# Kernel optimization log

Hardware: AMD Instinct MI355X
Metric: run time of the kernel (lower is better)

The kernel has to match this reference:

```python
import jax, jax.numpy as jnp
import numpy as np

NL, NQ, FD, HD, NH = 6, 128, 256, 512, 8
NC, B, T, H, W = 6, 1, 1, 48, 120
PPF = 24 // 6  # points_per_face
P = PPF * PPF * 6  # code emits (num_points//6)^2 points per face = 96 total
NPARAM, NTYPE, NATTR = 11, 10, 3
PMIN = np.array([-50., -50., -5., -15., -15., -5., -5., -3.14, 0.5, 0.5, 0.5], np.float32)
PMAX = np.array([50., 50., 5., 15., 15., 5., 5., 3.14, 10., 5., 3.], np.float32)


def _box_template():
    off = np.linspace(-0.4, 0.4, PPF).astype(np.float32)
    pts = []
    for axis in range(3):  # -x,+x,-y,+y,-z,+z faces, same order as torch code
        for s in (-0.5, 0.5):
            rem = [a for a in range(3) if a != axis]
            for i in range(PPF):
                for j in range(PPF):
                    p = [0.0, 0.0, 0.0]
                    p[axis] = s
                    p[rem[0]] = off[i]
                    p[rem[1]] = off[j]
                    pts.append(p)
    return np.asarray(pts, np.float32)  # [P,3]

TPL = _box_template()


def _mlp2(x, w1, b1, w2, b2):
    return jax.nn.relu(x @ w1.T + b1) @ w2.T + b2


def _ln(x, g, b):
    m = x.mean(-1, keepdims=True)
    v = ((x - m) ** 2).mean(-1, keepdims=True)
    return (x - m) * jax.lax.rsqrt(v + 1e-5) * g + b


def _mha(q, k, v, in_w, in_b, out_w, out_b):
    hd = HD // NH
    wq, wk, wv = jnp.split(in_w, 3, axis=0)
    bq, bk, bv = jnp.split(in_b, 3)
    def heads(x, w, b):
        y = x @ w.T + b
        return y.reshape(x.shape[0], x.shape[1], NH, hd).transpose(0, 2, 1, 3)
    Q, K, V = heads(q, wq, bq), heads(k, wk, bk), heads(v, wv, bv)
    a = jax.nn.softmax(jnp.einsum('bhqd,bhkd->bhqk', Q, K) * (hd ** -0.5), axis=-1)
    o = jnp.einsum('bhqk,bhkd->bhqd', a, V)
    o = o.transpose(0, 2, 1, 3).reshape(q.shape[0], q.shape[1], HD)
    return o @ out_w.T + out_b


def _sample_box_points(motion):
    # motion [B,N,11] -> [B,N,P,3]; indices: X0 Y1 Z2 .. YAW7 L8 W9 H10
    c = motion[..., 0:3]
    dims = motion[..., 8:11]
    yaw = motion[..., 7]
    p = TPL * dims[:, :, None, :]  # [B,N,P,3]
    cy, sy = jnp.cos(yaw)[..., None], jnp.sin(yaw)[..., None]
    xr = p[..., 0] * cy - p[..., 1] * sy
    yr = p[..., 0] * sy + p[..., 1] * cy
    return jnp.stack([xr, yr, p[..., 2]], -1) + c[:, :, None, :]


def _gather_aggregate(pts, features, proj):
    # pts [B,N,P,3]; features [NC,B,T,C,H,W]; proj [NC,3,4]
    Bb, N, Pp, _ = pts.shape
    NP = N * Pp
    hom = jnp.concatenate([pts, jnp.ones_like(pts[..., :1])], -1)
    feat_flat = features.reshape(NC, Bb, T, FD, H * W)
    acc = jnp.zeros((Bb, FD, NP), features.dtype)
    for cidx in range(NC):
        cam = jnp.einsum('ij,bnpj->bnpi', proj[cidx], hom)  # [B,N,P,3]
        z = cam[..., 2]
        zs = jnp.where(jnp.abs(z) > 1e-6, z, 1e-6)
        u = (cam[..., 0] / zs).reshape(Bb, NP)
        v = (cam[..., 1] / zs).reshape(Bb, NP)
        front = (z > 0).reshape(Bb, NP)
        u0, v0 = jnp.floor(u), jnp.floor(v)
        du, dv = u - u0, v - v0
        cam_acc = jnp.zeros((Bb, T, FD, NP), features.dtype)
        for (ui, vi, wgt) in ((u0, v0, (1 - du) * (1 - dv)),
                              (u0 + 1, v0, du * (1 - dv)),
                              (u0, v0 + 1, (1 - du) * dv),
                              (u0 + 1, v0 + 1, du * dv)):
            ok = front & (ui >= 0) & (ui <= W - 1) & (vi >= 0) & (vi <= H - 1)
            idx = (jnp.clip(vi, 0, H - 1) * W + jnp.clip(ui, 0, W - 1)).astype(jnp.int32)
            bidx = jnp.broadcast_to(idx[:, None, None, :], (Bb, T, FD, NP))
            g = jnp.take_along_axis(feat_flat[cidx], bidx, axis=-1)
            cam_acc = cam_acc + g * (wgt * ok)[:, None, None, :]
        acc = acc + cam_acc.mean(axis=1)  # mean over time
    agg = (acc / NC).reshape(Bb, FD, N, Pp).mean(-1)  # mean over cams and points
    return agg.transpose(0, 2, 1)  # [B,N,C]

_ga = jax.checkpoint(_gather_aggregate)


def _forward(features, proj, ego_states, queries0, param_min, param_max, motion_w1, motion_b1, motion_w2, motion_b2, type_w1, type_b1, type_w2, type_b2, attr_w1, attr_b1, attr_w2, attr_b2, fmlp_w1, fmlp_b1, fmlp_w2, fmlp_b2, sa_in_w, sa_in_b, sa_out_w, sa_out_b, fa_in_w, fa_in_b, fa_out_w, fa_out_b, ffn_w1, ffn_b1, ffn_w2, ffn_b2, ln1_g, ln1_b, ln2_g, ln2_b, ln3_g, ln3_b):
    Bb = features.shape[1]
    q = jnp.broadcast_to(queries0, (Bb, NQ, HD))
    preds = []
    for i in range(NL):
        motion = jax.nn.sigmoid(_mlp2(q, motion_w1, motion_b1, motion_w2, motion_b2)) * (param_max - param_min) + param_min
        tlog = _mlp2(q, type_w1, type_b1, type_w2, type_b2)
        attr = jax.nn.sigmoid(_mlp2(q, attr_w1, attr_b1, attr_w2, attr_b2))
        preds.append(jnp.concatenate([motion, tlog, attr], -1))
        if i == NL - 1:
            break  # last layer only predicts (layers[-1] unused, as in torch code)
        pts = _sample_box_points(motion)
        agg = _ga(pts, features, proj)
        feat_h = _mlp2(agg, fmlp_w1, fmlp_b1, fmlp_w2, fmlp_b2)
        x = _ln(q, ln1_g[i], ln1_b[i])
        x = x + _mha(x, x, x, sa_in_w[i], sa_in_b[i], sa_out_w[i], sa_out_b[i])
        x = _ln(x, ln2_g[i], ln2_b[i])
        x = x + _mha(x, feat_h, feat_h, fa_in_w[i], fa_in_b[i], fa_out_w[i], fa_out_b[i])
        x = _ln(x, ln3_g[i], ln3_b[i])
        q = x + _mlp2(x, ffn_w1[i], ffn_b1[i], ffn_w2[i], ffn_b2[i])
    return jnp.stack(preds)  # [NL,B,NQ,24]


def setup_inputs() -> dict:
    key = jax.random.key(0)
    ks = iter(jax.random.split(key, 64))
    def g(shape, s=0.02):
        return jax.random.normal(next(ks), shape, jnp.float32) * s
    fx, cx, cy = 40.0, W / 2.0, H / 2.0
    Ps = []
    for c in range(NC):
        th = 2.0 * np.pi * c / NC
        Rm = np.stack([np.array([-np.sin(th), np.cos(th), 0.0]),
                       np.array([0.0, 0.0, -1.0]),
                       np.array([np.cos(th), np.sin(th), 0.0])])
        K = np.array([[fx, 0.0, cx], [0.0, fx, cy], [0.0, 0.0, 1.0]])
        Pm = np.zeros((3, 4))
        Pm[:, :3] = K @ Rm
        Ps.append(Pm)
    inp = dict(
        features=jax.random.normal(next(ks), (NC, B, T, FD, H, W), jnp.float32),
        proj=jnp.asarray(np.asarray(Ps, np.float32)),
        ego_states=jax.random.normal(next(ks), (B, T, 5), jnp.float32),
        queries0=g((1, NQ, HD), 1.0),
        param_min=jnp.asarray(PMIN), param_max=jnp.asarray(PMAX),
        motion_w1=g((HD, HD)), motion_b1=jnp.zeros((HD,)),
        motion_w2=g((NPARAM, HD)), motion_b2=jnp.zeros((NPARAM,)),
        type_w1=g((HD, HD)), type_b1=jnp.zeros((HD,)),
        type_w2=g((NTYPE, HD)), type_b2=jnp.zeros((NTYPE,)),
        attr_w1=g((HD, HD)), attr_b1=jnp.zeros((HD,)),
        attr_w2=g((NATTR, HD)), attr_b2=jnp.zeros((NATTR,)),
        fmlp_w1=g((HD, FD)), fmlp_b1=jnp.zeros((HD,)),
        fmlp_w2=g((HD, HD)), fmlp_b2=jnp.zeros((HD,)),
        sa_in_w=g((NL, 3 * HD, HD)), sa_in_b=jnp.zeros((NL, 3 * HD)),
        sa_out_w=g((NL, HD, HD)), sa_out_b=jnp.zeros((NL, HD)),
        fa_in_w=g((NL, 3 * HD, HD)), fa_in_b=jnp.zeros((NL, 3 * HD)),
        fa_out_w=g((NL, HD, HD)), fa_out_b=jnp.zeros((NL, HD)),
        ffn_w1=g((NL, 4 * HD, HD)), ffn_b1=jnp.zeros((NL, 4 * HD)),
        ffn_w2=g((NL, HD, 4 * HD)), ffn_b2=jnp.zeros((NL, HD)),
        ln1_g=jnp.ones((NL, HD)), ln1_b=jnp.zeros((NL, HD)),
        ln2_g=jnp.ones((NL, HD)), ln2_b=jnp.zeros((NL, HD)),
        ln3_g=jnp.ones((NL, HD)), ln3_b=jnp.zeros((NL, HD)),
    )
    return inp


def reference(features, proj, ego_states, queries0, param_min, param_max, motion_w1, motion_b1, motion_w2, motion_b2, type_w1, type_b1, type_w2, type_b2, attr_w1, attr_b1, attr_w2, attr_b2, fmlp_w1, fmlp_b1, fmlp_w2, fmlp_b2, sa_in_w, sa_in_b, sa_out_w, sa_out_b, fa_in_w, fa_in_b, fa_out_w, fa_out_b, ffn_w1, ffn_b1, ffn_w2, ffn_b2, ln1_g, ln1_b, ln2_g, ln2_b, ln3_g, ln3_b):
    return _forward(features, proj, ego_states, queries0, param_min, param_max, motion_w1, motion_b1, motion_w2, motion_b2, type_w1, type_b1, type_w2, type_b2, attr_w1, attr_b1, attr_w2, attr_b2, fmlp_w1, fmlp_b1, fmlp_w2, fmlp_b2, sa_in_w, sa_in_b, sa_out_w, sa_out_b, fa_in_w, fa_in_b, fa_out_w, fa_out_b, ffn_w1, ffn_b1, ffn_w2, ffn_b2, ln1_g, ln1_b, ln2_g, ln2_b, ln3_g, ln3_b)
```

## Files before the change

kernel.cpp:

```cpp
#include <hip/hip_runtime.h>
#include <hip/hip_bf16.h>

typedef __hip_bfloat16 bf16;
typedef _Float16 h16;
typedef __attribute__((ext_vector_type(8))) _Float16 half8;
typedef __attribute__((ext_vector_type(4))) float f32x4;

#define NQ 128
#define HD 512
#define FD 256
#define NC 6
#define IMH 48
#define IMW 120
#define HW 5760

__device__ __forceinline__ half8 pack8(float4 x, float4 y) {
    half8 h;
    h[0] = (h16)x.x; h[1] = (h16)x.y; h[2] = (h16)x.z; h[3] = (h16)x.w;
    h[4] = (h16)y.x; h[5] = (h16)y.y; h[6] = (h16)y.z; h[7] = (h16)y.w;
    return h;
}

__global__ __launch_bounds__(256) void transpose_feat_k(const float* __restrict__ f,
                                                        bf16* __restrict__ ft)
{
    __shared__ float tile[32][33];
    int cam = blockIdx.z;
    int hw0 = blockIdx.x * 32, fd0 = blockIdx.y * 32;
    int tx = threadIdx.x, ty = threadIdx.y;
    const float* fb = f + (size_t)cam * FD * HW;
    for (int r = ty; r < 32; r += 8)
        tile[r][tx] = fb[(size_t)(fd0 + r) * HW + hw0 + tx];
    __syncthreads();
    bf16* fo = ft + (size_t)cam * HW * FD;
    for (int r = ty; r < 32; r += 8)
        fo[(size_t)(hw0 + r) * FD + fd0 + tx] = __float2bfloat16(tile[tx][r]);
}

__global__ __launch_bounds__(256) void cvt16_k(const float* __restrict__ src,
                                               h16* __restrict__ dst, int n)
{
    int i = blockIdx.x * 256 + threadIdx.x;
    if (i < n) dst[i] = (h16)src[i];
}

struct SwzDesc {
    const float* src[11];
    unsigned int chunkStart[12];
    unsigned int tileStart[11];
    int K[11];
};

__global__ __launch_bounds__(256) void swizzle2_k(SwzDesc d, h16* __restrict__ dst)
{
    __shared__ h16 fbuf[4096];
    int bid = blockIdx.x;
    int w = 0;
    while (bid >= (int)d.chunkStart[w + 1]) w++;
    int local = bid - (int)d.chunkStart[w];
    int Kk = d.K[w];
    int kc = Kk >> 6;
    int n64 = local / kc, kchunk = local - n64 * kc;
    int t = threadIdx.x;
    int r = t >> 2, q = t & 3;
    int ct = r >> 4, lr = r & 15;
    const float* srow = d.src[w] + (size_t)(n64 * 64 + r) * Kk + kchunk * 64;
#pragma unroll
    for (int p = 0; p < 4; p++) {
        int c = (q + p * 4) * 4;
        float4 u = *(const float4*)(srow + c);
        int ksl = c >> 5, kk = c & 31;
        h16* fp = &fbuf[(size_t)(((ksl * 4 + ct) * 64) + (kk >> 3) * 16 + lr) * 8 + (kk & 7)];
        fp[0] = (h16)u.x; fp[1] = (h16)u.y; fp[2] = (h16)u.z; fp[3] = (h16)u.w;
    }
    __syncthreads();
    int K32 = Kk >> 5;
#pragma unroll
    for (int i = 0; i < 2; i++) {
        int hidx = t + i * 256;
        int tl = hidx >> 6, within = hidx & 63;
        int ksl = tl >> 2, ctt = tl & 3;
        size_t tileg = (size_t)d.tileStart[w]
                     + ((size_t)n64 * K32 + (kchunk * 2 + ksl)) * 4 + ctt;
        *(half8*)(dst + tileg * 512 + within * 8) = *(const half8*)&fbuf[tl * 512 + within * 8];
    }
}

template<int CTN, int NSUM, bool A2SW, bool LNA>
__global__ __launch_bounds__(256) void gemm_sk4(
    const h16* __restrict__ A16, int lda, int sumStride,
    const float* __restrict__ A32,
    const float* __restrict__ lng, const float* __restrict__ lnb,
    float* __restrict__ lnout,
    const h16* __restrict__ A2_16, int a2Start,
    const h16* __restrict__ Wswz,
    const float* __restrict__ B0, const float* __restrict__ B1, const float* __restrict__ B2s,
    const float* __restrict__ R, int ldr,
    float* __restrict__ C32, h16* __restrict__ C16, int ldc,
    int K, int act)
{
    __shared__ float redu[CTN * 4 * 256];
    __shared__ float sst[64], sst2[64];
    int bx = blockIdx.x, by = blockIdx.y;
    int tid = threadIdx.x;
    int w = tid >> 6, l = tid & 63;
    int lr = l & 15, q4 = l >> 4;
    int m0 = by * 16;
    int n0 = bx * 16 * CTN;
    int row = m0 + lr;
    int K32 = K >> 5;
    int KQ = K32 >> 2;
    int ks0 = w * KQ;

    bool useA2 = A2SW && (bx >= a2Start);

    const float* arow32 = nullptr;
    float mean = 0.f, rstd = 1.f;
    if (LNA && !useA2) {
        arow32 = A32 + (size_t)row * K + q4 * 8;
        float s = 0.f, s2 = 0.f;
        for (int ks = ks0; ks < ks0 + KQ; ks++) {
            float4 u = *(const float4*)(arow32 + ks * 32);
            float4 v = *(const float4*)(arow32 + ks * 32 + 4);
            s  += u.x + u.y + u.z + u.w + v.x + v.y + v.z + v.w;
            s2 += u.x*u.x + u.y*u.y + u.z*u.z + u.w*u.w
                + v.x*v.x + v.y*v.y + v.z*v.z + v.w*v.w;
        }
        s  += __shfl_xor(s, 16);  s  += __shfl_xor(s, 32);
        s2 += __shfl_xor(s2, 16); s2 += __shfl_xor(s2, 32);
        if (q4 == 0) { sst[w * 16 + lr] = s; sst2[w * 16 + lr] = s2; }
        __syncthreads();
        float st = sst[lr] + sst[16 + lr] + sst[32 + lr] + sst[48 + lr];
        float st2 = sst2[lr] + sst2[16 + lr] + sst2[32 + lr] + sst2[48 + lr];
        mean = st * (1.0f / (float)K);
        float var = st2 * (1.0f / (float)K) - mean * mean;
        rstd = rsqrtf(var + 1e-5f);
    }

    const h16* arow16 = nullptr;
    if (useA2)       arow16 = A2_16 + (size_t)row * 512 + q4 * 8;
    else if (!LNA)   arow16 = A16 + (size_t)row * lda + q4 * 8;

    const h16* wbase[CTN];
#pragma unroll
    for (int ct = 0; ct < CTN; ct++) {
        int tct = (n0 >> 4) + ct;
        wbase[ct] = Wswz + (((size_t)(tct >> 2) * K32 * 4 + (tct & 3)) * 64 + l) * 8;
    }

    f32x4 acc[CTN];
#pragma unroll
    for (int ct = 0; ct < CTN; ct++) acc[ct] = (f32x4){0.f, 0.f, 0.f, 0.f};

    bool wrln = LNA && !useA2 && (bx == 0) && lnout;

#pragma unroll 4
    for (int ks = ks0; ks < ks0 + KQ; ks++) {
        half8 a;
        if (LNA && !useA2) {
            float4 u = *(const float4*)(arow32 + ks * 32);
            float4 v = *(const float4*)(arow32 + ks * 32 + 4);
            float4 g0 = *(const float4*)(lng + ks * 32 + q4 * 8);
            float4 g1 = *(const float4*)(lng + ks * 32 + q4 * 8 + 4);
            float4 b0 = *(const float4*)(lnb + ks * 32 + q4 * 8);
            float4 b1 = *(const float4*)(lnb + ks * 32 + q4 * 8 + 4);
            float4 o0, o1;
            o0.x = (u.x - mean) * rstd * g0.x + b0.x;
            o0.y = (u.y - mean) * rstd * g0.y + b0.y;
            o0.z = (u.z - mean) * rstd * g0.z + b0.z;
            o0.w = (u.w - mean) * rstd * g0.w + b0.w;
            o1.x = (v.x - mean) * rstd * g1.x + b1.x;
            o1.y = (v.y - mean) * rstd * g1.y + b1.y;
            o1.z = (v.z - mean) * rstd * g1.z + b1.z;
            o1.w = (v.w - mean) * rstd * g1.w + b1.w;
            if (wrln) {
                *(float4*)(lnout + (size_t)row * K + ks * 32 + q4 * 8)     = o0;
                *(float4*)(lnout + (size_t)row * K + ks * 32 + q4 * 8 + 4) = o1;
            }
            a = pack8(o0, o1);
        } else if (NSUM == 1) {
            a = *(const half8*)(arow16 + (size_t)ks * 32);
        } else {
            float s[8] = {0.f, 0.f, 0.f, 0.f, 0.f, 0.f, 0.f, 0.f};
#pragma unroll
            for (int j = 0; j < NSUM; j++) {
                half8 tt = *(const half8*)(arow16 + (size_t)j * sumStride + ks * 32);
#pragma unroll
                for (int e = 0; e < 8; e++) s[e] += (float)tt[e];
            }
#pragma unroll
            for (int e = 0; e < 8; e++) a[e] = (h16)s[e];
        }
#pragma unroll
        for (int ct = 0; ct < CTN; ct++) {
            half8 bfr = *(const half8*)(wbase[ct] + (size_t)ks * 2048);
            acc[ct] = __builtin_amdgcn_mfma_f32_16x16x32_f16(a, bfr, acc[ct], 0, 0, 0);
        }
    }

#pragma unroll
    for (int ct = 0; ct < CTN; ct++)
        *(f32x4*)&redu[(size_t)(w * CTN + ct) * 256 + l * 4] = acc[ct];
    __syncthreads();

    if (w < CTN) {
        int ct = w;
        f32x4 sum = *(const f32x4*)&redu[(size_t)ct * 256 + l * 4];
#pragma unroll
        for (int w2 = 1; w2 < 4; w2++) {
            f32x4 tt = *(const f32x4*)&redu[(size_t)(w2 * CTN + ct) * 256 + l * 4];
            sum[0] += tt[0]; sum[1] += tt[1]; sum[2] += tt[2]; sum[3] += tt[3];
        }
        int n = n0 + ct * 16 + lr;
        float bv;
        if (B1) { int sec = n >> 9, ni = n & 511;
                  bv = (sec == 0) ? B0[ni] : (sec == 1 ? B1[ni] : B2s[ni]); }
        else bv = B0[n];
#pragma unroll
        for (int r = 0; r < 4; r++) {
            int m = m0 + q4 * 4 + r;
            float v = sum[r] + bv;
            if (act) v = fmaxf(v, 0.f);
            if (R) v += R[(size_t)m * ldr + n];
            if (C32) C32[(size_t)m * ldc + n] = v;
            if (C16) C16[(size_t)m * ldc + n] = (h16)v;
        }
    }
}

__global__ __launch_bounds__(64) void heads2_k(const h16* __restrict__ hid16,
                                               const float* __restrict__ w2m, const float* __restrict__ b2m,
                                               const float* __restrict__ w2t, const float* __restrict__ b2t,
                                               const float* __restrict__ w2a, const float* __restrict__ b2a,
                                               const float* __restrict__ pmin, const float* __restrict__ pmax,
                                               float* __restrict__ out)
{
    int q = blockIdx.x, n = blockIdx.y, lane = threadIdx.x;
    const float* wr; float bv; int mode, sect;
    if (n < 11)      { sect = 0; wr = w2m + n * 512;        bv = b2m[n];      mode = 0; }
    else if (n < 21) { sect = 1; wr = w2t + (n - 11) * 512; bv = b2t[n - 11]; mode = 1; }
    else             { sect = 2; wr = w2a + (n - 21) * 512; bv = b2a[n - 21]; mode = 2; }
    half8 hv = *(const half8*)(hid16 + q * 1536 + sect * 512 + lane * 8);
    const float4* w4 = (const float4*)(wr + lane * 8);
    float4 c0 = w4[0], c1 = w4[1];
    float acc = (float)hv[0] * c0.x + (float)hv[1] * c0.y
              + (float)hv[2] * c0.z + (float)hv[3] * c0.w
              + (float)hv[4] * c1.x + (float)hv[5] * c1.y
              + (float)hv[6] * c1.z + (float)hv[7] * c1.w;
    for (int off = 32; off; off >>= 1) acc += __shfl_xor(acc, off);
    if (lane == 0) {
        float v = acc + bv;
        if (mode == 0)      v = (1.0f / (1.0f + __expf(-v))) * (pmax[n] - pmin[n]) + pmin[n];
        else if (mode == 2) v = 1.0f / (1.0f + __expf(-v));
        out[q * 24 + n] = v;
    }
}

__global__ __launch_bounds__(256) void attn_k(const float* __restrict__ qkv,
                                              h16* __restrict__ out16)
{
    __shared__ float KVl[128 * 68];
    __shared__ float Ql[32 * 68];
    __shared__ float Pl[32 * 128];
    int h = blockIdx.x >> 2, chunk = blockIdx.x & 3;
    int tid = threadIdx.x;

    for (int l = tid; l < 2048; l += 256) {
        int row = l >> 4, c4 = (l & 15) * 4;
        float4 v = *(const float4*)&qkv[row * 1536 + 512 + h * 64 + c4];
        *(float4*)&KVl[row * 68 + c4] = v;
    }
    for (int l = tid; l < 512; l += 256) {
        int row = l >> 4, c4 = (l & 15) * 4;
        float4 v = *(const float4*)&qkv[(chunk * 32 + row) * 1536 + h * 64 + c4];
        *(float4*)&Ql[row * 68 + c4] = v;
    }
    __syncthreads();

    int w = tid >> 6, j = tid & 63;
    for (int r8 = 0; r8 < 8; r8++) {
        int lr = w * 8 + r8;
        float s0 = 0.f, s1 = 0.f;
#pragma unroll
        for (int k4 = 0; k4 < 64; k4 += 4) {
            float4 qv  = *(const float4*)&Ql[lr * 68 + k4];
            float4 k0v = *(const float4*)&KVl[j * 68 + k4];
            float4 k1v = *(const float4*)&KVl[(j + 64) * 68 + k4];
            s0 += qv.x * k0v.x + qv.y * k0v.y + qv.z * k0v.z + qv.w * k0v.w;
            s1 += qv.x * k1v.x + qv.y * k1v.y + qv.z * k1v.z + qv.w * k1v.w;
        }
        s0 *= 0.125f; s1 *= 0.125f;
        float m = fmaxf(s0, s1);
        for (int off = 32; off; off >>= 1) m = fmaxf(m, __shfl_xor(m, off));
        float e0 = __expf(s0 - m), e1 = __expf(s1 - m);
        float sm = e0 + e1;
        for (int off = 32; off; off >>= 1) sm += __shfl_xor(sm, off);
        float inv = 1.0f / sm;
        Pl[lr * 128 + j]      = e0 * inv;
        Pl[lr * 128 + j + 64] = e1 * inv;
    }
    __syncthreads();

    for (int l = tid; l < 2048; l += 256) {
        int row = l >> 4, c4 = (l & 15) * 4;
        float4 v = *(const float4*)&qkv[row * 1536 + 1024 + h * 64 + c4];
        KVl[(c4 + 0) * 132 + row] = v.x;
        KVl[(c4 + 1) * 132 + row] = v.y;
        KVl[(c4 + 2) * 132 + row] = v.z;
        KVl[(c4 + 3) * 132 + row] = v.w;
    }
    __syncthreads();

    int d = tid & 63, w2 = tid >> 6;
    for (int r8 = 0; r8 < 8; r8++) {
        int lr = w2 * 8 + r8;
        float o = 0.f;
#pragma unroll
        for (int j4 = 0; j4 < 128; j4 += 4) {
            float4 pv = *(const float4*)&Pl[lr * 128 + j4];
            float4 vv = *(const float4*)&KVl[d * 132 + j4];
            o += pv.x * vv.x + pv.y * vv.y + pv.z * vv.z + pv.w * vv.w;
        }
        out16[(chunk * 32 + lr) * 512 + h * 64 + d] = (h16)o;
    }
}

__device__ __forceinline__ float bflo(unsigned u) {
    union { unsigned i; float f; } c; c.i = u << 16; return c.f;
}
__device__ __forceinline__ float bfhi(unsigned u) {
    union { unsigned i; float f; } c; c.i = u & 0xffff0000u; return c.f;
}

__global__ __launch_bounds__(256) void gather_k(const bf16* __restrict__ ft,
                                                const float* __restrict__ proj,
                                                const float* __restrict__ preds,
                                                h16* __restrict__ agg16)
{
    __shared__ float mo[11];
    __shared__ int   goff[384];
    __shared__ float gw[384];
    __shared__ int   cnt;
    __shared__ float part[8][256];
    int n = blockIdx.x, cam = blockIdx.y, tid = threadIdx.x;
    if (tid == 0) cnt = 0;
    if (tid < 11) mo[tid] = preds[n * 24 + tid];
    __syncthreads();

    if (tid < 96) {
        int p = tid;
        float dd0 = mo[8], dd1 = mo[9], dd2 = mo[10];
        float c0 = mo[0], c1 = mo[1], c2 = mo[2];
        float sy, cy;
        sincosf(mo[7], &sy, &cy);
        int face = p >> 4, axis = face >> 1;
        float sgn = (face & 1) ? 0.5f : -0.5f;
        float offi = -0.4f + (float)((p >> 2) & 3) * (0.8f / 3.0f);
        float offj = -0.4f + (float)(p & 3) * (0.8f / 3.0f);
        float t0, t1, t2;
        if (axis == 0)      { t0 = sgn;  t1 = offi; t2 = offj; }
        else if (axis == 1) { t0 = offi; t1 = sgn;  t2 = offj; }
        else                { t0 = offi; t1 = offj; t2 = sgn;  }
        float px = t0 * dd0, py = t1 * dd1, pz = t2 * dd2;
        float X = px * cy - py * sy + c0;
        float Y = px * sy + py * cy + c1;
        float Z = pz + c2;
        const float* P = proj + cam * 12;
        float cu = P[0] * X + P[1] * Y + P[2] * Z + P[3];
        float cv = P[4] * X + P[5] * Y + P[6] * Z + P[7];
        float cz = P[8] * X + P[9] * Y + P[10] * Z + P[11];
        float zs = (fabsf(cz) > 1e-6f) ? cz : 1e-6f;
        float u = cu / zs, v = cv / zs;
        bool front = cz > 0.0f;
        float u0 = floorf(u), v0 = floorf(v);
        float du = u - u0, dv = v - v0;
        float us[4] = {u0, u0 + 1.0f, u0, u0 + 1.0f};
        float vs[4] = {v0, v0, v0 + 1.0f, v0 + 1.0f};
        float wt[4] = {(1.0f - du) * (1.0f - dv), du * (1.0f - dv),
                       (1.0f - du) * dv, du * dv};
        int   myoff[4]; float myw[4]; int k = 0;
#pragma unroll
        for (int t = 0; t < 4; t++) {
            bool ok = front && (us[t] >= 0.0f) && (us[t] <= 119.0f)
                            && (vs[t] >= 0.0f) && (vs[t] <= 47.0f)
                            && (wt[t] > 0.0f);
            if (ok) {
                myoff[k] = ((int)vs[t] * IMW + (int)us[t]) * FD;
                myw[k]   = wt[t];
                k++;
            }
        }
        if (k) {
            int base = atomicAdd(&cnt, k);
            for (int s = 0; s < k; s++) { goff[base + s] = myoff[s]; gw[base + s] = myw[s]; }
        }
    }
    __syncthreads();
    int C = cnt;
    h16* slab = agg16 + (size_t)cam * 32768 + n * 256;
    if (C == 0) { slab[tid] = (h16)0.f; return; }

    int g8  = (tid & 31) * 8;
    int row = tid >> 5;
    const bf16* fb = ft + (size_t)cam * HW * FD + g8;
    float acc[8] = {0.f, 0.f, 0.f, 0.f, 0.f, 0.f, 0.f, 0.f};
    for (int e = row; e < C; e += 8) {
        float w = gw[e];
        uint4 rv = *(const uint4*)(fb + goff[e]);
        acc[0] += w * bflo(rv.x); acc[1] += w * bfhi(rv.x);
        acc[2] += w * bflo(rv.y); acc[3] += w * bfhi(rv.y);
        acc[4] += w * bflo(rv.z); acc[5] += w * bfhi(rv.z);
        acc[6] += w * bflo(rv.w); acc[7] += w * bfhi(rv.w);
    }
#pragma unroll
    for (int j = 0; j < 8; j++) part[row][g8 + j] = acc[j];
    __syncthreads();
    float s = 0.f;
#pragma unroll
    for (int r = 0; r < 8; r++) s += part[r][tid];
    slab[tid] = (h16)(s * (1.0f / 576.0f));
}

extern "C" void kernel_launch(void* const* d_in, const int* in_sizes, int n_in,
                              void* d_out, int out_size, void* d_ws, size_t ws_size,
                              hipStream_t stream)
{
    const float* features  = (const float*)d_in[0];
    const float* proj      = (const float*)d_in[1];
    const float* queries0  = (const float*)d_in[3];
    const float* pmin      = (const float*)d_in[4];
    const float* pmax      = (const float*)d_in[5];
    const float* motion_w1 = (const float*)d_in[6];
    const float* motion_b1 = (const float*)d_in[7];
    const float* motion_w2 = (const float*)d_in[8];
    const float* motion_b2 = (const float*)d_in[9];
    const float* type_w1   = (const float*)d_in[10];
    const float* type_b1   = (const float*)d_in[11];
    const float* type_w2   = (const float*)d_in[12];
    const float* type_b2   = (const float*)d_in[13];
    const float* attr_w1   = (const float*)d_in[14];
    const float* attr_b1   = (const float*)d_in[15];
    const float* attr_w2   = (const float*)d_in[16];
    const float* attr_b2   = (const float*)d_in[17];
    const float* fmlp_w1   = (const float*)d_in[18];
    const float* fmlp_b1   = (const float*)d_in[19];
    const float* fmlp_w2   = (const float*)d_in[20];
    const float* fmlp_b2   = (const float*)d_in[21];
    const float* sa_in_w   = (const float*)d_in[22];
    const float* sa_in_b   = (const float*)d_in[23];
    const float* sa_out_w  = (const float*)d_in[24];
    const float* sa_out_b  = (const float*)d_in[25];
    const float* fa_in_w   = (const float*)d_in[26];
    const float* fa_in_b   = (const float*)d_in[27];
    const float* fa_out_w  = (const float*)d_in[28];
    const float* fa_out_b  = (const float*)d_in[29];
    const float* ffn_w1    = (const float*)d_in[30];
    const float* ffn_b1    = (const float*)d_in[31];
    const float* ffn_w2    = (const float*)d_in[32];
    const float* ffn_b2    = (const float*)d_in[33];
    const float* ln1_g     = (const float*)d_in[34];
    const float* ln1_b     = (const float*)d_in[35];
    const float* ln2_g     = (const float*)d_in[36];
    const float* ln2_b     = (const float*)d_in[37];
    const float* ln3_g     = (const float*)d_in[38];
    const float* ln3_b     = (const float*)d_in[39];
    float* out = (float*)d_out;

    char* p = (char*)d_ws;
    bf16* feat_t = (bf16*)p;   p += (size_t)NC * HW * FD * 2;
    h16* swz     = (h16*)p;    p += (size_t)51456 * 512 * 2;
    h16* q016    = (h16*)p;    p += 65536 * 2;
    h16* hid16   = (h16*)p;    p += 196608 * 2;
    h16* agg16   = (h16*)p;    p += 196608 * 2;
    h16* fmlph16 = (h16*)p;    p += 65536 * 2;
    h16* feath16 = (h16*)p;    p += 65536 * 2;
    h16* attnb16 = (h16*)p;    p += 65536 * 2;
    h16* ffnh16  = (h16*)p;    p += 262144 * 2;
    h16* qn16    = (h16*)p;    p += 65536 * 2;
    float* qkv   = (float*)p;  p += 196608 * 4;
    float* lnx   = (float*)p;  p += 65536 * 4;
    float* x1    = (float*)p;  p += 65536 * 4;
    float* x2    = (float*)p;  p += 65536 * 4;
    float* qn32  = (float*)p;  p += 65536 * 4;

    SwzDesc sd;
    const float* srcs[11] = {motion_w1, type_w1, attr_w1, fmlp_w1, fmlp_w2,
                             sa_in_w, sa_out_w, fa_in_w, fa_out_w, ffn_w1, ffn_w2};
    int Ks[11]    = {512, 512, 512, 256, 512, 512, 512, 512, 512, 512, 2048};
    int tiles[11] = {512, 512, 512, 256, 512, 9216, 3072, 9216, 3072, 12288, 12288};
    unsigned int cumT = 0, cumC = 0;
    for (int i = 0; i < 11; i++) {
        sd.src[i] = srcs[i]; sd.K[i] = Ks[i];
        sd.tileStart[i] = cumT; sd.chunkStart[i] = cumC;
        cumT += tiles[i]; cumC += tiles[i] >> 3;
    }
    sd.chunkStart[11] = cumC;

    swizzle2_k<<<6432, 256, 0, stream>>>(sd, swz);
    cvt16_k<<<256, 256, 0, stream>>>(queries0, q016, 65536);
    transpose_feat_k<<<dim3(180, 8, 6), dim3(32, 8), 0, stream>>>(features, feat_t);

    const h16* sw_heads = swz;
    const h16* sw_fmlp1 = swz + 786432;
    const h16* sw_fmlp2 = swz + 917504;
    const h16* sw_sain  = swz + 1179648;
    const h16* sw_saout = swz + 5898240;
    const h16* sw_fain  = swz + 7471104;
    const h16* sw_faout = swz + 12189696;
    const h16* sw_ffn1  = swz + 13762560;
    const h16* sw_ffn2  = swz + 20054016;

    const h16*   q16 = q016;
    const float* q32 = queries0;

    for (int i = 0; i < 6; i++) {
        gemm_sk4<2, 1, false, false><<<dim3(48, 8), 256, 0, stream>>>(
            q16, 512, 0, nullptr, nullptr, nullptr, nullptr, nullptr, 0,
            sw_heads, motion_b1, type_b1, attr_b1, nullptr, 0,
            nullptr, hid16, 1536, 512, 1);
        heads2_k<<<dim3(128, 24), 64, 0, stream>>>(hid16, motion_w2, motion_b2,
                                                   type_w2, type_b2, attr_w2, attr_b2,
                                                   pmin, pmax, out + i * 3072);
        if (i == 5) break;

        gather_k<<<dim3(128, 6), 256, 0, stream>>>(feat_t, proj, out + i * 3072, agg16);
        gemm_sk4<1, 6, false, false><<<dim3(32, 8), 256, 0, stream>>>(
            agg16, 256, 32768, nullptr, nullptr, nullptr, nullptr, nullptr, 0,
            sw_fmlp1, fmlp_b1, nullptr, nullptr, nullptr, 0,
            nullptr, fmlph16, 512, 256, 1);
        gemm_sk4<1, 1, false, false><<<dim3(32, 8), 256, 0, stream>>>(
            fmlph16, 512, 0, nullptr, nullptr, nullptr, nullptr, nullptr, 0,
            sw_fmlp2, fmlp_b2, nullptr, nullptr, nullptr, 0,
            nullptr, feath16, 512, 512, 0);

        gemm_sk4<2, 1, false, true><<<dim3(48, 8), 256, 0, stream>>>(
            nullptr, 0, 0, q32, ln1_g + i * 512, ln1_b + i * 512, lnx, nullptr, 0,
            sw_sain + (size_t)i * 786432, sa_in_b + i * 1536, nullptr, nullptr,
            nullptr, 0, qkv, nullptr, 1536, 512, 0);
        attn_k<<<32, 256, 0, stream>>>(qkv, attnb16);
        gemm_sk4<1, 1, false, false><<<dim3(32, 8), 256, 0, stream>>>(
            attnb16, 512, 0, nullptr, nullptr, nullptr, nullptr, nullptr, 0,
            sw_saout + (size_t)i * 262144, sa_out_b + i * 512, nullptr, nullptr,
            lnx, 512, x1, nullptr, 512, 512, 0);

        gemm_sk4<2, 1, true, true><<<dim3(48, 8), 256, 0, stream>>>(
            nullptr, 0, 0, x1, ln2_g + i * 512, ln2_b + i * 512, lnx, feath16, 16,
            sw_fain + (size_t)i * 786432, fa_in_b + i * 1536, nullptr, nullptr,
            nullptr, 0, qkv, nullptr, 1536, 512, 0);
        attn_k<<<32, 256, 0, stream>>>(qkv, attnb16);
        gemm_sk4<1, 1, false, false><<<dim3(32, 8), 256, 0, stream>>>(
            attnb16, 512, 0, nullptr, nullptr, nullptr, nullptr, nullptr, 0,
            sw_faout + (size_t)i * 262144, fa_out_b + i * 512, nullptr, nullptr,
            lnx, 512, x2, nullptr, 512, 512, 0);

        gemm_sk4<2, 1, false, true><<<dim3(64, 8), 256, 0, stream>>>(
            nullptr, 0, 0, x2, ln3_g + i * 512, ln3_b + i * 512, lnx, nullptr, 0,
            sw_ffn1 + (size_t)i * 1048576, ffn_b1 + i * 2048, nullptr, nullptr,
            nullptr, 0, nullptr, ffnh16, 2048, 512, 1);
        gemm_sk4<1, 1, false, false><<<dim3(32, 8), 256, 0, stream>>>(
            ffnh16, 2048, 0, nullptr, nullptr, nullptr, nullptr, nullptr, 0,
            sw_ffn2 + (size_t)i * 1048576, ffn_b2 + i * 512, nullptr, nullptr,
            lnx, 512, qn32, qn16, 512, 2048, 0);

        q16 = qn16;
        q32 = qn32;
    }
}
```

Measured before the change: 863.2 us.

## Drop weight pre-swizzle pass and read fp32 weights directly in GEMMs

Removes the upfront kernel that converted every weight matrix to fp16 in an MFMA-tiled layout. The GEMM now loads fp32 rows straight from the original weights and packs them to fp16 in registers. This saves one large conversion pass over all weights, but each GEMM reads twice the bytes with a less coalesced, row-strided pattern. Some weights are reused across the 6 iterations, so they are now converted repeatedly.

```diff
diff --git a/kernel.cpp b/kernel.cpp
--- a/kernel.cpp
+++ b/kernel.cpp
@@ -44,48 +44,6 @@
     if (i < n) dst[i] = (h16)src[i];
 }
 
-struct SwzDesc {
-    const float* src[11];
-    unsigned int chunkStart[12];
-    unsigned int tileStart[11];
-    int K[11];
-};
-
-__global__ __launch_bounds__(256) void swizzle2_k(SwzDesc d, h16* __restrict__ dst)
-{
-    __shared__ h16 fbuf[4096];
-    int bid = blockIdx.x;
-    int w = 0;
-    while (bid >= (int)d.chunkStart[w + 1]) w++;
-    int local = bid - (int)d.chunkStart[w];
-    int Kk = d.K[w];
-    int kc = Kk >> 6;
-    int n64 = local / kc, kchunk = local - n64 * kc;
-    int t = threadIdx.x;
-    int r = t >> 2, q = t & 3;
-    int ct = r >> 4, lr = r & 15;
-    const float* srow = d.src[w] + (size_t)(n64 * 64 + r) * Kk + kchunk * 64;
-#pragma unroll
-    for (int p = 0; p < 4; p++) {
-        int c = (q + p * 4) * 4;
-        float4 u = *(const float4*)(srow + c);
-        int ksl = c >> 5, kk = c & 31;
-        h16* fp = &fbuf[(size_t)(((ksl * 4 + ct) * 64) + (kk >> 3) * 16 + lr) * 8 + (kk & 7)];
-        fp[0] = (h16)u.x; fp[1] = (h16)u.y; fp[2] = (h16)u.z; fp[3] = (h16)u.w;
-    }
-    __syncthreads();
-    int K32 = Kk >> 5;
-#pragma unroll
-    for (int i = 0; i < 2; i++) {
-        int hidx = t + i * 256;
-        int tl = hidx >> 6, within = hidx & 63;
-        int ksl = tl >> 2, ctt = tl & 3;
-        size_t tileg = (size_t)d.tileStart[w]
-                     + ((size_t)n64 * K32 + (kchunk * 2 + ksl)) * 4 + ctt;
-        *(half8*)(dst + tileg * 512 + within * 8) = *(const half8*)&fbuf[tl * 512 + within * 8];
-    }
-}
-
 template<int CTN, int NSUM, bool A2SW, bool LNA>
 __global__ __launch_bounds__(256) void gemm_sk4(
     const h16* __restrict__ A16, int lda, int sumStride,
@@ -93,7 +51,7 @@
     const float* __restrict__ lng, const float* __restrict__ lnb,
     float* __restrict__ lnout,
     const h16* __restrict__ A2_16, int a2Start,
-    const h16* __restrict__ Wswz,
+    const float* __restrict__ W0f, const float* __restrict__ W1f, const float* __restrict__ W2f,
     const float* __restrict__ B0, const float* __restrict__ B1, const float* __restrict__ B2s,
     const float* __restrict__ R, int ldr,
     float* __restrict__ C32, h16* __restrict__ C16, int ldc,
@@ -141,11 +99,18 @@
     if (useA2)       arow16 = A2_16 + (size_t)row * 512 + q4 * 8;
     else if (!LNA)   arow16 = A16 + (size_t)row * lda + q4 * 8;
 
-    const h16* wbase[CTN];
+    const float* wrow[CTN];
 #pragma unroll
     for (int ct = 0; ct < CTN; ct++) {
-        int tct = (n0 >> 4) + ct;
-        wbase[ct] = Wswz + (((size_t)(tct >> 2) * K32 * 4 + (tct & 3)) * 64 + l) * 8;
+        int nb = n0 + ct * 16;
+        const float* ws;
+        if (W1f) {
+            int sec = nb >> 9, ni = nb & 511;
+            ws = (sec == 0 ? W0f : (sec == 1 ? W1f : W2f)) + (size_t)ni * K;
+        } else {
+            ws = W0f + (size_t)nb * K;
+        }
+        wrow[ct] = ws + (size_t)lr * K + q4 * 8;
     }
 
     f32x4 acc[CTN];
@@ -193,7 +158,10 @@
         }
 #pragma unroll
         for (int ct = 0; ct < CTN; ct++) {
-            half8 bfr = *(const half8*)(wbase[ct] + (size_t)ks * 2048);
+            const float* wp = wrow[ct] + (size_t)ks * 32;
+            float4 wu = *(const float4*)(wp);
+            float4 wv = *(const float4*)(wp + 4);
+            half8 bfr = pack8(wu, wv);
             acc[ct] = __builtin_amdgcn_mfma_f32_16x16x32_f16(a, bfr, acc[ct], 0, 0, 0);
         }
     }
@@ -468,7 +436,6 @@
 
     char* p = (char*)d_ws;
     bf16* feat_t = (bf16*)p;   p += (size_t)NC * HW * FD * 2;
-    h16* swz     = (h16*)p;    p += (size_t)51456 * 512 * 2;
     h16* q016    = (h16*)p;    p += 65536 * 2;
     h16* hid16   = (h16*)p;    p += 196608 * 2;
     h16* agg16   = (h16*)p;    p += 196608 * 2;
@@ -483,32 +450,8 @@
     float* x2    = (float*)p;  p += 65536 * 4;
     float* qn32  = (float*)p;  p += 65536 * 4;
 
-    SwzDesc sd;
-    const float* srcs[11] = {motion_w1, type_w1, attr_w1, fmlp_w1, fmlp_w2,
-                             sa_in_w, sa_out_w, fa_in_w, fa_out_w, ffn_w1, ffn_w2};
-    int Ks[11]    = {512, 512, 512, 256, 512, 512, 512, 512, 512, 512, 2048};
-    int tiles[11] = {512, 512, 512, 256, 512, 9216, 3072, 9216, 3072, 12288, 12288};
-    unsigned int cumT = 0, cumC = 0;
-    for (int i = 0; i < 11; i++) {
-        sd.src[i] = srcs[i]; sd.K[i] = Ks[i];
-        sd.tileStart[i] = cumT; sd.chunkStart[i] = cumC;
-        cumT += tiles[i]; cumC += tiles[i] >> 3;
-    }
-    sd.chunkStart[11] = cumC;
-
-    swizzle2_k<<<6432, 256, 0, stream>>>(sd, swz);
     cvt16_k<<<256, 256, 0, stream>>>(queries0, q016, 65536);
     transpose_feat_k<<<dim3(180, 8, 6), dim3(32, 8), 0, stream>>>(features, feat_t);
-
-    const h16* sw_heads = swz;
-    const h16* sw_fmlp1 = swz + 786432;
-    const h16* sw_fmlp2 = swz + 917504;
-    const h16* sw_sain  = swz + 1179648;
-    const h16* sw_saout = swz + 5898240;
-    const h16* sw_fain  = swz + 7471104;
-    const h16* sw_faout = swz + 12189696;
-    const h16* sw_ffn1  = swz + 13762560;
-    const h16* sw_ffn2  = swz + 20054016;
 
     const h16*   q16 = q016;
     const float* q32 = queries0;
@@ -516,7 +459,8 @@
     for (int i = 0; i < 6; i++) {
         gemm_sk4<2, 1, false, false><<<dim3(48, 8), 256, 0, stream>>>(
             q16, 512, 0, nullptr, nullptr, nullptr, nullptr, nullptr, 0,
-            sw_heads, motion_b1, type_b1, attr_b1, nullptr, 0,
+            motion_w1, type_w1, attr_w1,
+            motion_b1, type_b1, attr_b1, nullptr, 0,
             nullptr, hid16, 1536, 512, 1);
         heads2_k<<<dim3(128, 24), 64, 0, stream>>>(hid16, motion_w2, motion_b2,
                                                    type_w2, type_b2, attr_w2, attr_b2,
@@ -526,40 +470,48 @@
         gather_k<<<dim3(128, 6), 256, 0, stream>>>(feat_t, proj, out + i * 3072, agg16);
         gemm_sk4<1, 6, false, false><<<dim3(32, 8), 256, 0, stream>>>(
             agg16, 256, 32768, nullptr, nullptr, nullptr, nullptr, nullptr, 0,
-            sw_fmlp1, fmlp_b1, nullptr, nullptr, nullptr, 0,
+            fmlp_w1, nullptr, nullptr,
+            fmlp_b1, nullptr, nullptr, nullptr, 0,
             nullptr, fmlph16, 512, 256, 1);
         gemm_sk4<1, 1, false, false><<<dim3(32, 8), 256, 0, stream>>>(
             fmlph16, 512, 0, nullptr, nullptr, nullptr, nullptr, nullptr, 0,
-            sw_fmlp2, fmlp_b2, nullptr, nullptr, nullptr, 0,
+            fmlp_w2, nullptr, nullptr,
+            fmlp_b2, nullptr, nullptr, nullptr, 0,
             nullptr, feath16, 512, 512, 0);
 
         gemm_sk4<2, 1, false, true><<<dim3(48, 8), 256, 0, stream>>>(
             nullptr, 0, 0, q32, ln1_g + i * 512, ln1_b + i * 512, lnx, nullptr, 0,
-            sw_sain + (size_t)i * 786432, sa_in_b + i * 1536, nullptr, nullptr,
+            sa_in_w + (size_t)i * 1536 * 512, nullptr, nullptr,
+            sa_in_b + i * 1536, nullptr, nullptr,
             nullptr, 0, qkv, nullptr, 1536, 512, 0);
         attn_k<<<32, 256, 0, stream>>>(qkv, attnb16);
         gemm_sk4<1, 1, false, false><<<dim3(32, 8), 256, 0, stream>>>(
             attnb16, 512, 0, nullptr, nullptr, nullptr, nullptr, nullptr, 0,
-            sw_saout + (size_t)i * 262144, sa_out_b + i * 512, nullptr, nullptr,
+            sa_out_w + (size_t)i * 512 * 512, nullptr, nullptr,
+            sa_out_b + i * 512, nullptr, nullptr,
             lnx, 512, x1, nullptr, 512, 512, 0);
 
         gemm_sk4<2, 1, true, true><<<dim3(48, 8), 256, 0, stream>>>(
             nullptr, 0, 0, x1, ln2_g + i * 512, ln2_b + i * 512, lnx, feath16, 16,
-            sw_fain + (size_t)i * 786432, fa_in_b + i * 1536, nullptr, nullptr,
+            fa_in_w + (size_t)i * 1536 * 512, nullptr, nullptr,
+            fa_in_b + i * 1536, nullptr, nullptr,
             nullptr, 0, qkv, nullptr, 1536, 512, 0);
         attn_k<<<32, 256, 0, stream>>>(qkv, attnb16);
         gemm_sk4<1, 1, false, false><<<dim3(32, 8), 256, 0, stream>>>(
             attnb16, 512, 0, nullptr, nullptr, nullptr, nullptr, nullptr, 0,
-            sw_faout + (size_t)i * 262144, fa_out_b + i * 512, nullptr, nullptr,
+            fa_out_w + (size_t)i * 512 * 512, nullptr, nullptr,
+            fa_out_b + i * 512, nullptr, nullptr,
             lnx, 512, x2, nullptr, 512, 512, 0);
 
         gemm_sk4<2, 1, false, true><<<dim3(64, 8), 256, 0, stream>>>(
             nullptr, 0, 0, x2, ln3_g + i * 512, ln3_b + i * 512, lnx, nullptr, 0,
-            sw_ffn1 + (size_t)i * 1048576, ffn_b1 + i * 2048, nullptr, nullptr,
+            ffn_w1 + (size_t)i * 2048 * 512, nullptr, nullptr,
+            ffn_b1 + i * 2048, nullptr, nullptr,
             nullptr, 0, nullptr, ffnh16, 2048, 512, 1);
         gemm_sk4<1, 1, false, false><<<dim3(32, 8), 256, 0, stream>>>(
             ffnh16, 2048, 0, nullptr, nullptr, nullptr, nullptr, nullptr, 0,
-            sw_ffn2 + (size_t)i * 1048576, ffn_b2 + i * 512, nullptr, nullptr,
+            ffn_w2 + (size_t)i * 512 * 2048, nullptr, nullptr,
+            ffn_b2 + i * 512, nullptr, nullptr,
             lnx, 512, qn32, qn16, 512, 2048, 0);
 
         q16 = qn16;
```

Result: slower. 936.1 us (+8.4%).
